# Optimization experiments

Hardware: AMD Instinct MI355X
Metric: run time of the kernel (lower is better)

## Reference

```python
import jax, jax.numpy as jnp
import numpy as np

N_NODES = 100000
N_EDGES = 1600000
F_IN = 128      # dataset.num_features
HID = 128       # hidden_dim (heads=1)
HID_POST = 128  # hidden_dim_post
EDGE_DIM = 16
N_CLASSES = 16
NEG_SLOPE = 0.2  # PyG GATConv default leaky_relu slope


def setup_inputs() -> dict:
    key = jax.random.key(0)
    ks = jax.random.split(key, 16)
    s = 0.1  # weight scale
    inp = {
        "x": jax.random.normal(ks[0], (N_NODES, F_IN), jnp.float32),
        "edge_attr": jax.random.normal(ks[1], (N_EDGES, EDGE_DIM), jnp.float32),
        "W0": jax.random.normal(ks[2], (F_IN, HID), jnp.float32) * s,
        "a_src0": jax.random.normal(ks[3], (HID,), jnp.float32) * s,
        "a_dst0": jax.random.normal(ks[4], (HID,), jnp.float32) * s,
        "We0": jax.random.normal(ks[5], (EDGE_DIM, HID), jnp.float32) * s,
        "a_e0": jax.random.normal(ks[6], (HID,), jnp.float32) * s,
        "b0": jnp.zeros((HID,), jnp.float32),
        "W1": jax.random.normal(ks[7], (HID, HID), jnp.float32) * s,
        "a_src1": jax.random.normal(ks[8], (HID,), jnp.float32) * s,
        "a_dst1": jax.random.normal(ks[9], (HID,), jnp.float32) * s,
        "We1": jax.random.normal(ks[10], (EDGE_DIM, HID), jnp.float32) * s,
        "a_e1": jax.random.normal(ks[11], (HID,), jnp.float32) * s,
        "b1": jnp.zeros((HID,), jnp.float32),
        "lin1_w": jax.random.normal(ks[12], (HID, HID_POST), jnp.float32) * s,
        "lin1_b": jnp.zeros((HID_POST,), jnp.float32),
        "lin2_w": jax.random.normal(ks[13], (HID_POST, N_CLASSES), jnp.float32) * s,
        "lin2_b": jnp.zeros((N_CLASSES,), jnp.float32),
        "edge_index": jax.random.randint(ks[14], (2, N_EDGES), 0, N_NODES, jnp.int64),
    }
    return inp


def gat_conv(x, src, dst, edge_attr, W, a_s, a_d, We, a_e, b):
    """PyG GATConv, heads=1, edge_dim set, add_self_loops=True (fill_value='mean')."""
    n = x.shape[0]
    xl = x @ W                       # [N, HID] shared lin for src/dst
    alpha_src_n = xl @ a_s           # [N]
    alpha_dst_n = xl @ a_d           # [N]
    # self loops: edge_attr filled with per-target-node mean of incoming edge_attr
    deg = jax.ops.segment_sum(jnp.ones(src.shape[0], x.dtype), dst, num_segments=n)
    ea_mean = jax.ops.segment_sum(edge_attr, dst, num_segments=n) / jnp.maximum(deg, 1.0)[:, None]
    loop = jnp.arange(n, dtype=src.dtype)
    src_f = jnp.concatenate([src, loop])
    dst_f = jnp.concatenate([dst, loop])
    ea_f = jnp.concatenate([edge_attr, ea_mean], axis=0)  # [E+N, EDGE_DIM]
    alpha_edge = (ea_f @ We) @ a_e                        # [E+N]
    alpha = jax.nn.leaky_relu(
        alpha_src_n[src_f] + alpha_dst_n[dst_f] + alpha_edge, NEG_SLOPE
    )
    # segment softmax over destination node (every node has its self loop -> nonempty)
    amax = jax.ops.segment_max(alpha, dst_f, num_segments=n)
    ex = jnp.exp(alpha - amax[dst_f])
    denom = jax.ops.segment_sum(ex, dst_f, num_segments=n)
    w = ex / denom[dst_f]                                 # [E+N]
    out = jax.ops.segment_sum(xl[src_f] * w[:, None], dst_f, num_segments=n)
    return out + b


def reference(x, edge_attr, W0, a_src0, a_dst0, We0, a_e0, b0,
              W1, a_src1, a_dst1, We1, a_e1, b1,
              lin1_w, lin1_b, lin2_w, lin2_b, edge_index):
    src, dst = edge_index[0], edge_index[1]
    # dropout layers are identity in eval mode
    h = jax.nn.relu(gat_conv(x, src, dst, edge_attr, W0, a_src0, a_dst0, We0, a_e0, b0))
    h = jax.nn.relu(gat_conv(h, src, dst, edge_attr, W1, a_src1, a_dst1, We1, a_e1, b1))
    h = jax.nn.relu(h @ lin1_w + lin1_b)
    logits = h @ lin2_w + lin2_b
    return jax.nn.log_softmax(logits, axis=-1)
```

## Files before the change

kernel.cpp:

```cpp
#include <hip/hip_runtime.h>
#include <math.h>

#define N_NODES 100000
#define N_EDGES 1600000
#define NEG 0.2f
#define MAXDEG 128
#define WPB 4

__device__ __forceinline__ float lrelu(float x){ return x > 0.f ? x : NEG*x; }
__device__ __forceinline__ unsigned short f2bf(float f){
  unsigned int u = __float_as_uint(f);
  u += 0x7FFFu + ((u >> 16) & 1u);
  return (unsigned short)(u >> 16);
}

__global__ __launch_bounds__(256) void k_pre(const int* __restrict__ dst, const float* __restrict__ eatt,
    const float* __restrict__ We0, const float* __restrict__ ae0,
    const float* __restrict__ We1, const float* __restrict__ ae1,
    int* __restrict__ deg, int* __restrict__ rank, float2* __restrict__ ae01,
    const float* __restrict__ X, const float* __restrict__ W,
    const float* __restrict__ a_s, const float* __restrict__ a_d,
    unsigned short* __restrict__ Ybf, float* __restrict__ asrc, float* __restrict__ adst){
  __shared__ float Xs[16][68];
  __shared__ float Ws[16][128];
  __shared__ float as_s[128], ad_s[128];
  int t = threadIdx.x;
  int bid = blockIdx.x;
  int rem = bid % 5;
  if (rem != 4){
    float* wea = &Ws[0][0];
    if (t < 32){
      const float* Wm = (t < 16) ? We0 : We1;
      const float* am = (t < 16) ? ae0 : ae1;
      int r = t & 15;
      float acc = 0.f;
      #pragma unroll
      for (int j=0;j<128;j++) acc += Wm[r*128+j]*am[j];
      wea[t] = acc;
    }
    __syncthreads();
    int e = ((bid/5)*4 + rem)*256 + t;
    if (e >= N_EDGES) return;
    const float4* p = (const float4*)(eatt + (size_t)e*16);
    float4 a0=p[0], a1=p[1], a2=p[2], a3=p[3];
    float f0 = a0.x*wea[0] +a0.y*wea[1] +a0.z*wea[2] +a0.w*wea[3]
             + a1.x*wea[4] +a1.y*wea[5] +a1.z*wea[6] +a1.w*wea[7]
             + a2.x*wea[8] +a2.y*wea[9] +a2.z*wea[10]+a2.w*wea[11]
             + a3.x*wea[12]+a3.y*wea[13]+a3.z*wea[14]+a3.w*wea[15];
    float f1 = a0.x*wea[16]+a0.y*wea[17]+a0.z*wea[18]+a0.w*wea[19]
             + a1.x*wea[20]+a1.y*wea[21]+a1.z*wea[22]+a1.w*wea[23]
             + a2.x*wea[24]+a2.y*wea[25]+a2.z*wea[26]+a2.w*wea[27]
             + a3.x*wea[28]+a3.y*wea[29]+a3.z*wea[30]+a3.w*wea[31];
    rank[e] = atomicAdd(&deg[dst[e]], 1);
    ae01[e] = make_float2(f0, f1);
    return;
  }
  if (t < 128){ as_s[t] = a_s[t]; ad_s[t] = a_d[t]; }
  int row0 = (bid/5) * 64;
  int tc = t & 15, tr = t >> 4;
  int c0 = tc*8, r0 = tr*4;
  int lr = t >> 2, lc = (t & 3) << 2;
  int wk = t >> 4, wc = (t & 15) * 8;
  float acc[4][8];
  #pragma unroll
  for (int i=0;i<4;i++)
    #pragma unroll
    for (int j=0;j<8;j++) acc[i][j]=0.f;
  int gr = row0 + lr;
  for (int k0=0; k0<128; k0+=16){
    float4 xv = make_float4(0.f,0.f,0.f,0.f);
    if (gr < N_NODES) xv = *(const float4*)(X + (size_t)gr*128 + k0 + lc);
    float4 wv0 = *(const float4*)(W + (size_t)(k0+wk)*128 + wc);
    float4 wv1 = *(const float4*)(W + (size_t)(k0+wk)*128 + wc + 4);
    __syncthreads();
    Xs[lc+0][lr]=xv.x; Xs[lc+1][lr]=xv.y; Xs[lc+2][lr]=xv.z; Xs[lc+3][lr]=xv.w;
    *(float4*)&Ws[wk][wc]   = wv0;
    *(float4*)&Ws[wk][wc+4] = wv1;
    __syncthreads();
    #pragma unroll
    for (int kk=0;kk<16;kk++){
      float4 a  = *(const float4*)&Xs[kk][r0];
      float4 b0 = *(const float4*)&Ws[kk][c0];
      float4 b1 = *(const float4*)&Ws[kk][c0+4];
      float av[4] = {a.x,a.y,a.z,a.w};
      float bv[8] = {b0.x,b0.y,b0.z,b0.w,b1.x,b1.y,b1.z,b1.w};
      #pragma unroll
      for (int i=0;i<4;i++)
        #pragma unroll
        for (int j=0;j<8;j++) acc[i][j] += av[i]*bv[j];
    }
  }
  #pragma unroll
  for (int i=0;i<4;i++){
    int r = row0 + r0 + i;
    float v[8];
    #pragma unroll
    for (int j=0;j<8;j++) v[j] = acc[i][j];
    if (r < N_NODES){
      uint4 pk;
      pk.x = (unsigned)f2bf(v[0]) | ((unsigned)f2bf(v[1])<<16);
      pk.y = (unsigned)f2bf(v[2]) | ((unsigned)f2bf(v[3])<<16);
      pk.z = (unsigned)f2bf(v[4]) | ((unsigned)f2bf(v[5])<<16);
      pk.w = (unsigned)f2bf(v[6]) | ((unsigned)f2bf(v[7])<<16);
      *(uint4*)(Ybf + (size_t)r*128 + c0) = pk;
    }
    float s=0.f, d=0.f;
    #pragma unroll
    for (int j=0;j<8;j++){ s += v[j]*as_s[c0+j]; d += v[j]*ad_s[c0+j]; }
    #pragma unroll
    for (int off=1; off<16; off<<=1){ s += __shfl_xor(s,off); d += __shfl_xor(d,off); }
    if ((t & 15)==0 && r < N_NODES){ asrc[r]=s; adst[r]=d; }
  }
}

__global__ __launch_bounds__(256) void k_scan_a(const int* __restrict__ deg, int* __restrict__ incl, int* __restrict__ bsum){
  __shared__ int s[256];
  int t = threadIdx.x; int i = blockIdx.x*256 + t;
  int v = (i < N_NODES) ? deg[i] : 0;
  s[t] = v; __syncthreads();
  for (int off=1; off<256; off<<=1){
    int u = (t>=off)? s[t-off] : 0; __syncthreads();
    s[t] += u; __syncthreads();
  }
  if (i < N_NODES) incl[i] = s[t];
  if (t == 255) bsum[blockIdx.x] = s[t];
}
__global__ __launch_bounds__(512) void k_scan_b(const int* __restrict__ bsum, int* __restrict__ bexcl, int nb){
  __shared__ int s[512];
  int t = threadIdx.x;
  int v = (t<nb)? bsum[t] : 0;
  s[t] = v; __syncthreads();
  for (int off=1; off<512; off<<=1){
    int u = (t>=off)? s[t-off] : 0; __syncthreads();
    s[t] += u; __syncthreads();
  }
  if (t<nb) bexcl[t] = s[t]-v;
}
__global__ __launch_bounds__(256) void k_scan_c(const int* __restrict__ incl, const int* __restrict__ deg,
    const int* __restrict__ bexcl, int* __restrict__ rowptr){
  int i = blockIdx.x*256+threadIdx.x;
  if (i < N_NODES) rowptr[i] = incl[i] - deg[i] + bexcl[blockIdx.x];
  if (i == 0) rowptr[N_NODES] = N_EDGES;
}

__global__ __launch_bounds__(256) void k_fillf(const int* __restrict__ src, const int* __restrict__ dst,
     const int* __restrict__ rank, const float2* __restrict__ ae01,
     const int* __restrict__ rowptr, uint4* __restrict__ csr){
  int e = blockIdx.x*256+threadIdx.x;
  if (e >= N_EDGES) return;
  int d = dst[e];
  float2 ae = ae01[e];
  int pos = rowptr[d] + rank[e];
  csr[pos] = make_uint4((unsigned)src[e], __float_as_uint(ae.x), __float_as_uint(ae.y), 0u);
}

__global__ __launch_bounds__(256) void k_gemm(const float* __restrict__ X, const float* __restrict__ W,
    const float* __restrict__ bias, float* __restrict__ Y, unsigned short* __restrict__ Ybf,
    const float* __restrict__ a_s, const float* __restrict__ a_d,
    float* __restrict__ asrc, float* __restrict__ adst, int M, int relu){
  __shared__ float Xs[16][68];
  __shared__ float Ws[16][128];
  __shared__ float as_s[128], ad_s[128];
  int t = threadIdx.x;
  if (a_s && t < 128){ as_s[t] = a_s[t]; ad_s[t] = a_d[t]; }
  int row0 = blockIdx.x * 64;
  int tc = t & 15, tr = t >> 4;
  int c0 = tc*8, r0 = tr*4;
  int lr = t >> 2, lc = (t & 3) << 2;
  int wk = t >> 4, wc = (t & 15) * 8;
  float acc[4][8];
  #pragma unroll
  for (int i=0;i<4;i++)
    #pragma unroll
    for (int j=0;j<8;j++) acc[i][j]=0.f;
  int gr = row0 + lr;
  for (int k0=0; k0<128; k0+=16){
    float4 xv = make_float4(0.f,0.f,0.f,0.f);
    if (gr < M) xv = *(const float4*)(X + (size_t)gr*128 + k0 + lc);
    float4 wv0 = *(const float4*)(W + (size_t)(k0+wk)*128 + wc);
    float4 wv1 = *(const float4*)(W + (size_t)(k0+wk)*128 + wc + 4);
    __syncthreads();
    Xs[lc+0][lr]=xv.x; Xs[lc+1][lr]=xv.y; Xs[lc+2][lr]=xv.z; Xs[lc+3][lr]=xv.w;
    *(float4*)&Ws[wk][wc]   = wv0;
    *(float4*)&Ws[wk][wc+4] = wv1;
    __syncthreads();
    #pragma unroll
    for (int kk=0;kk<16;kk++){
      float4 a  = *(const float4*)&Xs[kk][r0];
      float4 b0 = *(const float4*)&Ws[kk][c0];
      float4 b1 = *(const float4*)&Ws[kk][c0+4];
      float av[4] = {a.x,a.y,a.z,a.w};
      float bv[8] = {b0.x,b0.y,b0.z,b0.w,b1.x,b1.y,b1.z,b1.w};
      #pragma unroll
      for (int i=0;i<4;i++)
        #pragma unroll
        for (int j=0;j<8;j++) acc[i][j] += av[i]*bv[j];
    }
  }
  #pragma unroll
  for (int i=0;i<4;i++){
    int r = row0 + r0 + i;
    float v[8];
    #pragma unroll
    for (int j=0;j<8;j++){
      float u = acc[i][j] + (bias ? bias[c0+j] : 0.f);
      v[j] = relu ? fmaxf(u, 0.f) : u;
    }
    if (r < M){
      if (Y){
        *(float4*)(Y + (size_t)r*128 + c0)     = make_float4(v[0],v[1],v[2],v[3]);
        *(float4*)(Y + (size_t)r*128 + c0 + 4) = make_float4(v[4],v[5],v[6],v[7]);
      }
      if (Ybf){
        uint4 pk;
        pk.x = (unsigned)f2bf(v[0]) | ((unsigned)f2bf(v[1])<<16);
        pk.y = (unsigned)f2bf(v[2]) | ((unsigned)f2bf(v[3])<<16);
        pk.z = (unsigned)f2bf(v[4]) | ((unsigned)f2bf(v[5])<<16);
        pk.w = (unsigned)f2bf(v[6]) | ((unsigned)f2bf(v[7])<<16);
        *(uint4*)(Ybf + (size_t)r*128 + c0) = pk;
      }
    }
    if (a_s){
      float s=0.f, d=0.f;
      #pragma unroll
      for (int j=0;j<8;j++){ s += v[j]*as_s[c0+j]; d += v[j]*ad_s[c0+j]; }
      #pragma unroll
      for (int off=1; off<16; off<<=1){ s += __shfl_xor(s,off); d += __shfl_xor(d,off); }
      if ((t & 15)==0 && r < M){ asrc[r]=s; adst[r]=d; }
    }
  }
}

__global__ __launch_bounds__(256) void k_agg(const int* __restrict__ rowptr, const uint4* __restrict__ csr,
    const float* __restrict__ asrc, const float* __restrict__ adst,
    const unsigned short* __restrict__ xlbf,
    const float* __restrict__ bias, float* __restrict__ out, int relu, int layer){
  int w = threadIdx.x >> 6;
  int lane = threadIdx.x & 63;
  int n = blockIdx.x * WPB + w;
  __shared__ float2 eb[WPB][MAXDEG];
  const char* xbase = (const char*)xlbf;
  int s0 = rowptr[n], s1 = rowptr[n+1];
  int deg = s1 - s0;
  float adst_n = adst[n];
  float m_edge = -1e30f;
  float sae = 0.f;
  for (int base=0; base<deg; base+=64){
    int i = base + lane;
    float a = -1e30f;
    if (i < deg){
      uint4 p4 = csr[s0 + i];
      int sx = (int)p4.x;
      float ae = __uint_as_float(layer ? p4.z : p4.y);
      float av = lrelu(asrc[sx] + adst_n + ae);
      if (i < MAXDEG) eb[w][i] = make_float2(av, __uint_as_float((unsigned)sx << 8));
      a = av;
      sae += ae;
    }
    for (int off=32; off; off>>=1) a = fmaxf(a, __shfl_xor(a, off));
    m_edge = fmaxf(m_edge, a);
  }
  for (int off=32; off; off>>=1) sae += __shfl_xor(sae, off);
  float aloop_n = sae / fmaxf((float)deg, 1.f);
  float al = lrelu(asrc[n] + adst_n + aloop_n);
  float m = fmaxf(m_edge, al);
  float p = 0.f;
  for (int i=lane; i<deg; i+=64){
    float av;
    if (i < MAXDEG) av = eb[w][i].x;
    else { uint4 p4 = csr[s0+i];
           av = lrelu(asrc[p4.x] + adst_n + __uint_as_float(layer ? p4.z : p4.y)); }
    float ev = __expf(av - m);
    if (i < MAXDEG) eb[w][i].x = ev;
    p += ev;
  }
  for (int off=32; off; off>>=1) p += __shfl_xor(p, off);
  float wl = __expf(al - m);
  float denom = p + wl;
  __syncthreads();
  int g = lane >> 4, cl = lane & 15;
  unsigned clb = (unsigned)(cl << 4);
  float acc[8];
  #pragma unroll
  for (int j=0;j<8;j++) acc[j]=0.f;
  if (g == 0){
    uint4 v = *(const uint4*)(xbase + (((unsigned)n << 8) + clb));
    unsigned int uu[4] = {v.x,v.y,v.z,v.w};
    #pragma unroll
    for (int q=0;q<4;q++){
      acc[2*q]   += wl * __uint_as_float(uu[q] << 16);
      acc[2*q+1] += wl * __uint_as_float(uu[q] & 0xFFFF0000u);
    }
  }
  if (deg <= MAXDEG){
    int dfull = deg & ~7;
    for (int i=0; i<dfull; i+=8){
      float2 e0 = eb[w][i+g];
      float2 e1 = eb[w][i+4+g];
      uint4 v0 = *(const uint4*)(xbase + (__float_as_uint(e0.y) + clb));
      uint4 v1 = *(const uint4*)(xbase + (__float_as_uint(e1.y) + clb));
      unsigned int uu0[4] = {v0.x,v0.y,v0.z,v0.w};
      unsigned int uu1[4] = {v1.x,v1.y,v1.z,v1.w};
      #pragma unroll
      for (int q=0;q<4;q++){
        acc[2*q]   += e0.x * __uint_as_float(uu0[q] << 16);
        acc[2*q+1] += e0.x * __uint_as_float(uu0[q] & 0xFFFF0000u);
      }
      #pragma unroll
      for (int q=0;q<4;q++){
        acc[2*q]   += e1.x * __uint_as_float(uu1[q] << 16);
        acc[2*q+1] += e1.x * __uint_as_float(uu1[q] & 0xFFFF0000u);
      }
    }
    for (int i=dfull; i<deg; i+=4){
      int idx = i + g;
      float we = 0.f; unsigned off = (unsigned)n << 8;
      if (idx < deg){ float2 e = eb[w][idx]; we = e.x; off = __float_as_uint(e.y); }
      uint4 v = *(const uint4*)(xbase + (off + clb));
      unsigned int uu[4] = {v.x,v.y,v.z,v.w};
      #pragma unroll
      for (int q=0;q<4;q++){
        acc[2*q]   += we * __uint_as_float(uu[q] << 16);
        acc[2*q+1] += we * __uint_as_float(uu[q] & 0xFFFF0000u);
      }
    }
  } else {
    for (int i=0; i<deg; i+=8){
      int idx0 = i + g, idx1 = i + 4 + g;
      int sx0 = n, sx1 = n; float we0 = 0.f, we1 = 0.f;
      if (idx0 < deg){
        if (idx0 < MAXDEG){ float2 e = eb[w][idx0]; we0 = e.x; sx0 = (int)(__float_as_uint(e.y) >> 8); }
        else { uint4 p4 = csr[s0+idx0]; sx0 = (int)p4.x;
               we0 = __expf(lrelu(asrc[sx0] + adst_n + __uint_as_float(layer ? p4.z : p4.y)) - m); }
      }
      if (idx1 < deg){
        if (idx1 < MAXDEG){ float2 e = eb[w][idx1]; we1 = e.x; sx1 = (int)(__float_as_uint(e.y) >> 8); }
        else { uint4 p4 = csr[s0+idx1]; sx1 = (int)p4.x;
               we1 = __expf(lrelu(asrc[sx1] + adst_n + __uint_as_float(layer ? p4.z : p4.y)) - m); }
      }
      uint4 v0 = *(const uint4*)(xbase + (((unsigned)sx0 << 8) + clb));
      uint4 v1 = *(const uint4*)(xbase + (((unsigned)sx1 << 8) + clb));
      unsigned int uu0[4] = {v0.x,v0.y,v0.z,v0.w};
      unsigned int uu1[4] = {v1.x,v1.y,v1.z,v1.w};
      #pragma unroll
      for (int q=0;q<4;q++){
        acc[2*q]   += we0 * __uint_as_float(uu0[q] << 16);
        acc[2*q+1] += we0 * __uint_as_float(uu0[q] & 0xFFFF0000u);
      }
      #pragma unroll
      for (int q=0;q<4;q++){
        acc[2*q]   += we1 * __uint_as_float(uu1[q] << 16);
        acc[2*q+1] += we1 * __uint_as_float(uu1[q] & 0xFFFF0000u);
      }
    }
  }
  #pragma unroll
  for (int j=0;j<8;j++){
    acc[j] += __shfl_xor(acc[j], 16);
    acc[j] += __shfl_xor(acc[j], 32);
  }
  if (lane < 16){
    float inv = 1.f/denom;
    float4 b0 = *(const float4*)(bias + cl*8);
    float4 b1 = *(const float4*)(bias + cl*8 + 4);
    float o[8];
    o[0]=acc[0]*inv+b0.x; o[1]=acc[1]*inv+b0.y; o[2]=acc[2]*inv+b0.z; o[3]=acc[3]*inv+b0.w;
    o[4]=acc[4]*inv+b1.x; o[5]=acc[5]*inv+b1.y; o[6]=acc[6]*inv+b1.z; o[7]=acc[7]*inv+b1.w;
    if (relu){
      #pragma unroll
      for (int j=0;j<8;j++) o[j]=fmaxf(o[j],0.f);
    }
    *(float4*)(out + (size_t)n*128 + cl*8)     = make_float4(o[0],o[1],o[2],o[3]);
    *(float4*)(out + (size_t)n*128 + cl*8 + 4) = make_float4(o[4],o[5],o[6],o[7]);
  }
}

__global__ __launch_bounds__(256) void k_mlp(const float* __restrict__ X, const float* __restrict__ W,
    const float* __restrict__ bias, const float* __restrict__ w2, const float* __restrict__ b2,
    float* __restrict__ out, int M){
  __shared__ float Xs[16][68];
  __shared__ float Ws[16][128];
  __shared__ float b2s[16];
  int t = threadIdx.x;
  int row0 = blockIdx.x * 64;
  int tc = t & 15, tr = t >> 4;
  int c0 = tc*8, r0 = tr*4;
  int lr = t >> 2, lc = (t & 3) << 2;
  int wk = t >> 4, wc = (t & 15) * 8;
  float acc[4][8];
  #pragma unroll
  for (int i=0;i<4;i++)
    #pragma unroll
    for (int j=0;j<8;j++) acc[i][j]=0.f;
  int gr = row0 + lr;
  for (int k0=0; k0<128; k0+=16){
    float4 xv = make_float4(0.f,0.f,0.f,0.f);
    if (gr < M) xv = *(const float4*)(X + (size_t)gr*128 + k0 + lc);
    float4 wv0 = *(const float4*)(W + (size_t)(k0+wk)*128 + wc);
    float4 wv1 = *(const float4*)(W + (size_t)(k0+wk)*128 + wc + 4);
    __syncthreads();
    Xs[lc+0][lr]=xv.x; Xs[lc+1][lr]=xv.y; Xs[lc+2][lr]=xv.z; Xs[lc+3][lr]=xv.w;
    *(float4*)&Ws[wk][wc]   = wv0;
    *(float4*)&Ws[wk][wc+4] = wv1;
    __syncthreads();
    #pragma unroll
    for (int kk=0;kk<16;kk++){
      float4 a  = *(const float4*)&Xs[kk][r0];
      float4 b0 = *(const float4*)&Ws[kk][c0];
      float4 b1 = *(const float4*)&Ws[kk][c0+4];
      float av[4] = {a.x,a.y,a.z,a.w};
      float bv[8] = {b0.x,b0.y,b0.z,b0.w,b1.x,b1.y,b1.z,b1.w};
      #pragma unroll
      for (int i=0;i<4;i++)
        #pragma unroll
        for (int j=0;j<8;j++) acc[i][j] += av[i]*bv[j];
    }
  }
  __syncthreads();
  float* wflat = &Ws[0][0];
  #pragma unroll
  for (int i=0;i<2;i++) ((float4*)wflat)[t + i*256] = ((const float4*)w2)[t + i*256];
  if (t < 16) b2s[t] = b2[t];
  float4 bba = *(const float4*)(bias + c0);
  float4 bbb = *(const float4*)(bias + c0 + 4);
  float bb[8] = {bba.x,bba.y,bba.z,bba.w,bbb.x,bbb.y,bbb.z,bbb.w};
  #pragma unroll
  for (int i=0;i<4;i++)
    #pragma unroll
    for (int j=0;j<8;j++) acc[i][j] = fmaxf(acc[i][j] + bb[j], 0.f);
  __syncthreads();
  float A0=0.f, A1=0.f, A2=0.f, A3=0.f;
  int sl = (tc+1) & 15;
  #pragma unroll 4
  for (int s=0; s<16; s++){
    int cls = (tc + s) & 15;
    const float* wp = wflat + (size_t)c0*16 + cls;
    float p0=0.f,p1=0.f,p2=0.f,p3=0.f;
    #pragma unroll
    for (int j=0;j<8;j++){
      float wv = wp[j*16];
      p0 += acc[0][j]*wv; p1 += acc[1][j]*wv; p2 += acc[2][j]*wv; p3 += acc[3][j]*wv;
    }
    A0+=p0; A1+=p1; A2+=p2; A3+=p3;
    A0=__shfl(A0,sl,16); A1=__shfl(A1,sl,16); A2=__shfl(A2,sl,16); A3=__shfl(A3,sl,16);
  }
  float A[4] = {A0,A1,A2,A3};
  float bcls = b2s[tc];
  #pragma unroll
  for (int i=0;i<4;i++){
    float v = A[i] + bcls;
    float m = v;
    #pragma unroll
    for (int off=1; off<16; off<<=1) m = fmaxf(m, __shfl_xor(m, off, 16));
    float ex = __expf(v - m);
    float sum = ex;
    #pragma unroll
    for (int off=1; off<16; off<<=1) sum += __shfl_xor(sum, off, 16);
    float lse = m + __logf(sum);
    int r = row0 + r0 + i;
    if (r < M) out[(size_t)r*16 + tc] = v - lse;
  }
}

extern "C" void kernel_launch(void* const* d_in, const int* in_sizes, int n_in,
                              void* d_out, int out_size, void* d_ws, size_t ws_size,
                              hipStream_t stream){
  const float* x    = (const float*)d_in[0];
  const float* eatt = (const float*)d_in[1];
  const float* W0   = (const float*)d_in[2];
  const float* as0  = (const float*)d_in[3];
  const float* ad0  = (const float*)d_in[4];
  const float* We0  = (const float*)d_in[5];
  const float* ae0  = (const float*)d_in[6];
  const float* b0   = (const float*)d_in[7];
  const float* W1   = (const float*)d_in[8];
  const float* as1  = (const float*)d_in[9];
  const float* ad1  = (const float*)d_in[10];
  const float* We1  = (const float*)d_in[11];
  const float* ae1  = (const float*)d_in[12];
  const float* b1   = (const float*)d_in[13];
  const float* l1w  = (const float*)d_in[14];
  const float* l1b  = (const float*)d_in[15];
  const float* l2w  = (const float*)d_in[16];
  const float* l2b  = (const float*)d_in[17];
  const int*   ei   = (const int*)d_in[18];
  const int* srcI = ei;
  const int* dstI = ei + N_EDGES;
  float* out = (float*)d_out;

  char* p = (char*)d_ws;
  auto alloc = [&](size_t bytes)->char*{ char* r = p; p += (bytes + 255) & ~255ull; return r; };
  unsigned short* Abf = (unsigned short*)alloc((size_t)N_NODES*128*2);
  float* B       = (float*)alloc((size_t)N_NODES*128*4);
  float* asrc    = (float*)alloc((size_t)N_NODES*4);
  float* adst    = (float*)alloc((size_t)N_NODES*4);
  int* deg     = (int*)alloc((size_t)N_NODES*4);
  int* rowptr  = (int*)alloc((size_t)(N_NODES+1)*4);
  uint4* csr   = (uint4*)alloc((size_t)N_EDGES*16);
  int* incl    = (int*)alloc((size_t)N_NODES*4);
  int* bsum    = (int*)alloc(512*4);
  int* bexcl   = (int*)alloc(512*4);
  char*   Bc   = (char*)B;
  int*    rank = (int*)Bc;
  float2* ae01 = (float2*)(Bc + 6400000);

  const int NB_E = (N_EDGES+255)/256;
  const int NB_N = (N_NODES+255)/256;
  const int NB_W = N_NODES/WPB;
  const int NB_G = (N_NODES+63)/64;
  const int NB_P = 7815;

  hipMemsetAsync(deg, 0, (size_t)N_NODES*4, stream);
  k_pre  <<<NB_P,256,0,stream>>>(dstI, eatt, We0, ae0, We1, ae1, deg, rank, ae01,
                                 x, W0, as0, ad0, Abf, asrc, adst);
  k_scan_a<<<NB_N,256,0,stream>>>(deg, incl, bsum);
  k_scan_b<<<1,  512,0,stream>>>(bsum, bexcl, NB_N);
  k_scan_c<<<NB_N,256,0,stream>>>(incl, deg, bexcl, rowptr);
  k_fillf <<<NB_E,256,0,stream>>>(srcI, dstI, rank, ae01, rowptr, csr);

  k_agg  <<<NB_W,256,0,stream>>>(rowptr, csr, asrc, adst, Abf, b0, B, 1, 0);

  k_gemm <<<NB_G,256,0,stream>>>(B, W1, nullptr, nullptr, Abf, as1, ad1, asrc, adst, N_NODES, 0);
  k_agg  <<<NB_W,256,0,stream>>>(rowptr, csr, asrc, adst, Abf, b1, B, 1, 1);

  k_mlp  <<<NB_G,256,0,stream>>>(B, l1w, l1b, l2w, l2b, out, N_NODES);
}
```

Baseline: 602.1 us.

## Rebalance fused prep kernel: two edges per thread, 32-row GEMM tiles

The fused preprocessing kernel now interleaves edge blocks and GEMM blocks 1:1 instead of 4:1. Edge blocks process two edges per thread (512 per block), and GEMM blocks compute 32-row tiles with a 2x8 per-thread micro-tile. Bounds checks are dropped because the node and edge counts divide the new tile sizes exactly. The grid shrinks to 6250 blocks. The aim is to balance the two block types and raise memory-level parallelism in the edge pass, at the cost of less register reuse per GEMM thread and more redundant loads of W across tiles.

Result: slower. 644.6 us (+7.1%).

```diff
diff --git a/kernel.cpp b/kernel.cpp
--- a/kernel.cpp
+++ b/kernel.cpp
@@ -21,13 +21,12 @@
     const float* __restrict__ X, const float* __restrict__ W,
     const float* __restrict__ a_s, const float* __restrict__ a_d,
     unsigned short* __restrict__ Ybf, float* __restrict__ asrc, float* __restrict__ adst){
-  __shared__ float Xs[16][68];
+  __shared__ float Xs[16][36];
   __shared__ float Ws[16][128];
   __shared__ float as_s[128], ad_s[128];
   int t = threadIdx.x;
   int bid = blockIdx.x;
-  int rem = bid % 5;
-  if (rem != 4){
+  if ((bid & 1) == 0){
     float* wea = &Ws[0][0];
     if (t < 32){
       const float* Wm = (t < 16) ? We0 : We1;
@@ -39,77 +38,88 @@
       wea[t] = acc;
     }
     __syncthreads();
-    int e = ((bid/5)*4 + rem)*256 + t;
-    if (e >= N_EDGES) return;
-    const float4* p = (const float4*)(eatt + (size_t)e*16);
-    float4 a0=p[0], a1=p[1], a2=p[2], a3=p[3];
-    float f0 = a0.x*wea[0] +a0.y*wea[1] +a0.z*wea[2] +a0.w*wea[3]
-             + a1.x*wea[4] +a1.y*wea[5] +a1.z*wea[6] +a1.w*wea[7]
-             + a2.x*wea[8] +a2.y*wea[9] +a2.z*wea[10]+a2.w*wea[11]
-             + a3.x*wea[12]+a3.y*wea[13]+a3.z*wea[14]+a3.w*wea[15];
-    float f1 = a0.x*wea[16]+a0.y*wea[17]+a0.z*wea[18]+a0.w*wea[19]
-             + a1.x*wea[20]+a1.y*wea[21]+a1.z*wea[22]+a1.w*wea[23]
-             + a2.x*wea[24]+a2.y*wea[25]+a2.z*wea[26]+a2.w*wea[27]
-             + a3.x*wea[28]+a3.y*wea[29]+a3.z*wea[30]+a3.w*wea[31];
-    rank[e] = atomicAdd(&deg[dst[e]], 1);
-    ae01[e] = make_float2(f0, f1);
+    int e0 = (bid >> 1)*512 + t;
+    int e1 = e0 + 256;
+    const float4* pa = (const float4*)(eatt + (size_t)e0*16);
+    const float4* pb = (const float4*)(eatt + (size_t)e1*16);
+    float4 a0=pa[0], a1=pa[1], a2=pa[2], a3=pa[3];
+    float4 b0=pb[0], b1=pb[1], b2=pb[2], b3=pb[3];
+    float f0a = a0.x*wea[0] +a0.y*wea[1] +a0.z*wea[2] +a0.w*wea[3]
+              + a1.x*wea[4] +a1.y*wea[5] +a1.z*wea[6] +a1.w*wea[7]
+              + a2.x*wea[8] +a2.y*wea[9] +a2.z*wea[10]+a2.w*wea[11]
+              + a3.x*wea[12]+a3.y*wea[13]+a3.z*wea[14]+a3.w*wea[15];
+    float f1a = a0.x*wea[16]+a0.y*wea[17]+a0.z*wea[18]+a0.w*wea[19]
+              + a1.x*wea[20]+a1.y*wea[21]+a1.z*wea[22]+a1.w*wea[23]
+              + a2.x*wea[24]+a2.y*wea[25]+a2.z*wea[26]+a2.w*wea[27]
+              + a3.x*wea[28]+a3.y*wea[29]+a3.z*wea[30]+a3.w*wea[31];
+    float f0b = b0.x*wea[0] +b0.y*wea[1] +b0.z*wea[2] +b0.w*wea[3]
+              + b1.x*wea[4] +b1.y*wea[5] +b1.z*wea[6] +b1.w*wea[7]
+              + b2.x*wea[8] +b2.y*wea[9] +b2.z*wea[10]+b2.w*wea[11]
+              + b3.x*wea[12]+b3.y*wea[13]+b3.z*wea[14]+b3.w*wea[15];
+    float f1b = b0.x*wea[16]+b0.y*wea[17]+b0.z*wea[18]+b0.w*wea[19]
+              + b1.x*wea[20]+b1.y*wea[21]+b1.z*wea[22]+b1.w*wea[23]
+              + b2.x*wea[24]+b2.y*wea[25]+b2.z*wea[26]+b2.w*wea[27]
+              + b3.x*wea[28]+b3.y*wea[29]+b3.z*wea[30]+b3.w*wea[31];
+    int da = dst[e0], db = dst[e1];
+    int ra = atomicAdd(&deg[da], 1);
+    int rb = atomicAdd(&deg[db], 1);
+    rank[e0] = ra;
+    rank[e1] = rb;
+    ae01[e0] = make_float2(f0a, f1a);
+    ae01[e1] = make_float2(f0b, f1b);
     return;
   }
   if (t < 128){ as_s[t] = a_s[t]; ad_s[t] = a_d[t]; }
-  int row0 = (bid/5) * 64;
+  int row0 = (bid >> 1) * 32;
   int tc = t & 15, tr = t >> 4;
-  int c0 = tc*8, r0 = tr*4;
-  int lr = t >> 2, lc = (t & 3) << 2;
+  int c0 = tc*8, r0 = tr*2;
+  int lr = (t & 127) >> 2, lc = (t & 3) << 2;
   int wk = t >> 4, wc = (t & 15) * 8;
-  float acc[4][8];
-  #pragma unroll
-  for (int i=0;i<4;i++)
+  float acc[2][8];
+  #pragma unroll
+  for (int i=0;i<2;i++)
     #pragma unroll
     for (int j=0;j<8;j++) acc[i][j]=0.f;
-  int gr = row0 + lr;
   for (int k0=0; k0<128; k0+=16){
     float4 xv = make_float4(0.f,0.f,0.f,0.f);
-    if (gr < N_NODES) xv = *(const float4*)(X + (size_t)gr*128 + k0 + lc);
+    if (t < 128) xv = *(const float4*)(X + (size_t)(row0+lr)*128 + k0 + lc);
     float4 wv0 = *(const float4*)(W + (size_t)(k0+wk)*128 + wc);
     float4 wv1 = *(const float4*)(W + (size_t)(k0+wk)*128 + wc + 4);
     __syncthreads();
-    Xs[lc+0][lr]=xv.x; Xs[lc+1][lr]=xv.y; Xs[lc+2][lr]=xv.z; Xs[lc+3][lr]=xv.w;
+    if (t < 128){
+      Xs[lc+0][lr]=xv.x; Xs[lc+1][lr]=xv.y; Xs[lc+2][lr]=xv.z; Xs[lc+3][lr]=xv.w;
+    }
     *(float4*)&Ws[wk][wc]   = wv0;
     *(float4*)&Ws[wk][wc+4] = wv1;
     __syncthreads();
     #pragma unroll
     for (int kk=0;kk<16;kk++){
-      float4 a  = *(const float4*)&Xs[kk][r0];
-      float4 b0 = *(const float4*)&Ws[kk][c0];
-      float4 b1 = *(const float4*)&Ws[kk][c0+4];
-      float av[4] = {a.x,a.y,a.z,a.w};
-      float bv[8] = {b0.x,b0.y,b0.z,b0.w,b1.x,b1.y,b1.z,b1.w};
-      #pragma unroll
-      for (int i=0;i<4;i++)
-        #pragma unroll
-        for (int j=0;j<8;j++) acc[i][j] += av[i]*bv[j];
-    }
-  }
-  #pragma unroll
-  for (int i=0;i<4;i++){
+      float a0v = Xs[kk][r0], a1v = Xs[kk][r0+1];
+      float4 wb0 = *(const float4*)&Ws[kk][c0];
+      float4 wb1 = *(const float4*)&Ws[kk][c0+4];
+      float bv[8] = {wb0.x,wb0.y,wb0.z,wb0.w,wb1.x,wb1.y,wb1.z,wb1.w};
+      #pragma unroll
+      for (int j=0;j<8;j++){ acc[0][j] += a0v*bv[j]; acc[1][j] += a1v*bv[j]; }
+    }
+  }
+  #pragma unroll
+  for (int i=0;i<2;i++){
     int r = row0 + r0 + i;
     float v[8];
     #pragma unroll
     for (int j=0;j<8;j++) v[j] = acc[i][j];
-    if (r < N_NODES){
-      uint4 pk;
-      pk.x = (unsigned)f2bf(v[0]) | ((unsigned)f2bf(v[1])<<16);
-      pk.y = (unsigned)f2bf(v[2]) | ((unsigned)f2bf(v[3])<<16);
-      pk.z = (unsigned)f2bf(v[4]) | ((unsigned)f2bf(v[5])<<16);
-      pk.w = (unsigned)f2bf(v[6]) | ((unsigned)f2bf(v[7])<<16);
-      *(uint4*)(Ybf + (size_t)r*128 + c0) = pk;
-    }
+    uint4 pk;
+    pk.x = (unsigned)f2bf(v[0]) | ((unsigned)f2bf(v[1])<<16);
+    pk.y = (unsigned)f2bf(v[2]) | ((unsigned)f2bf(v[3])<<16);
+    pk.z = (unsigned)f2bf(v[4]) | ((unsigned)f2bf(v[5])<<16);
+    pk.w = (unsigned)f2bf(v[6]) | ((unsigned)f2bf(v[7])<<16);
+    *(uint4*)(Ybf + (size_t)r*128 + c0) = pk;
     float s=0.f, d=0.f;
     #pragma unroll
     for (int j=0;j<8;j++){ s += v[j]*as_s[c0+j]; d += v[j]*ad_s[c0+j]; }
     #pragma unroll
     for (int off=1; off<16; off<<=1){ s += __shfl_xor(s,off); d += __shfl_xor(d,off); }
-    if ((t & 15)==0 && r < N_NODES){ asrc[r]=s; adst[r]=d; }
+    if ((t & 15)==0){ asrc[r]=s; adst[r]=d; }
   }
 }
 
@@ -508,7 +518,7 @@
   const int NB_N = (N_NODES+255)/256;
   const int NB_W = N_NODES/WPB;
   const int NB_G = (N_NODES+63)/64;
-  const int NB_P = 7815;
+  const int NB_P = 6250;
 
   hipMemsetAsync(deg, 0, (size_t)N_NODES*4, stream);
   k_pre  <<<NB_P,256,0,stream>>>(dstI, eatt, We0, ae0, We1, ae1, deg, rank, ae01,
```
